# Optimization experiments

Hardware: AMD Instinct MI355X
Metric: run time of the kernel (lower is better)

Reference implementation:

```python
import jax, jax.numpy as jnp
import numpy as np

K = 16  # number of neighbors (module init arg)

def setup_inputs() -> dict:
    key = jax.random.key(0)
    M, D, N = 65536, 16, 64
    x = jax.random.normal(key, (M, D), dtype=jnp.float32)
    # equal-length segments: each point set has M // N points
    segs = jnp.full((N,), M // N, dtype=jnp.int64)
    return {"x": x, "segs": segs}

def reference(x, segs):
    # Segmented kNN graph. Segments are equal-length (static shapes for jit),
    # so the per-segment pairwise distance + top-k becomes a batched op.
    B = segs.shape[0]
    M, D = x.shape
    L = M // B  # points per segment
    pts = x.reshape(B, L, D)
    # squared euclidean distances within each segment: (B, L, L)
    sq = jnp.sum(pts * pts, axis=-1)
    d2 = sq[:, :, None] + sq[:, None, :] - 2.0 * jnp.einsum('bld,bmd->blm', pts, pts)
    # k smallest distances per point (includes self, as in DGL's knn_graph)
    _, idx = jax.lax.top_k(-d2, K)  # idx: (B, L, K), local indices within segment
    offsets = (jnp.arange(B, dtype=idx.dtype) * L)[:, None, None]
    src = (idx + offsets).reshape(-1)                      # neighbor -> global node id
    dst = (jnp.arange(L, dtype=idx.dtype)[None, :, None] + offsets)  # (B, L, 1)
    dst = jnp.broadcast_to(dst, (B, L, K)).reshape(-1)
    # edges point from k-nearest neighbors (predecessors) to each node
    return src, dst
```

## Files before the change

### kernel.cpp

```cpp
#include <hip/hip_runtime.h>
#include <stdint.h>


#define L_SEG 1024
#define M_PTS 65536

typedef __fp16 fp16x2 __attribute__((ext_vector_type(2)));
typedef __fp16 fp16x4 __attribute__((ext_vector_type(4)));
typedef float  f32x4  __attribute__((ext_vector_type(4)));

__device__ __forceinline__ uint32_t umn(uint32_t a, uint32_t b) { return a < b ? a : b; }
__device__ __forceinline__ uint32_t umx(uint32_t a, uint32_t b) { return a > b ? a : b; }

#define CE(arr, i, p) { uint32_t lo = umn(arr[i], arr[p]); uint32_t hi = umx(arr[i], arr[p]); arr[i] = lo; arr[p] = hi; }

__device__ __forceinline__ void clean16(uint32_t* A) {
    #pragma unroll
    for (int j = 8; j > 0; j >>= 1) {
        #pragma unroll
        for (int i = 0; i < 16; ++i) {
            int p = i ^ j;
            if (p > i) CE(A, i, p);
        }
    }
}

__device__ __forceinline__ void sort16(uint32_t* B) {
    #pragma unroll
    for (int p = 1; p < 16; p <<= 1) {
        #pragma unroll
        for (int k = p; k >= 1; k >>= 1) {
            #pragma unroll
            for (int j = (k & (p - 1)); j + k < 16; j += 2 * k) {
                #pragma unroll
                for (int i = 0; i <= ((k - 1 < 15 - j - k) ? k - 1 : 15 - j - k); ++i) {
                    if ((i + j) / (2 * p) == (i + j + k) / (2 * p)) CE(B, i + j, i + j + k);
                }
            }
        }
    }
}

__device__ __forceinline__ void keep16(uint32_t* A, const uint32_t* S) {
    #pragma unroll
    for (int i = 0; i < 16; ++i) A[i] = umn(A[i], S[15 - i]);
    clean16(A);
}

__device__ __forceinline__ void mergeg(uint32_t* A) {
    #pragma unroll
    for (int m = 16; m <= 32; m <<= 1) {
        uint32_t P[16];
        #pragma unroll
        for (int i = 0; i < 16; ++i) P[i] = (uint32_t)__shfl_xor((int)A[15 - i], m, 64);
        #pragma unroll
        for (int i = 0; i < 16; ++i) A[i] = umn(A[i], P[i]);
        clean16(A);
    }
}

__device__ __forceinline__ uint32_t sel4(const uint32_t* A, int g, int v) {
    uint32_t t01 = (g & 1) ? A[4 + v]  : A[v];
    uint32_t t23 = (g & 1) ? A[12 + v] : A[8 + v];
    return (g & 2) ? t23 : t01;
}

__global__ __launch_bounds__(512, 6) void knn_v10_kernel(const float* __restrict__ x,
                                                         int* __restrict__ out) {
    __shared__ __attribute__((aligned(16))) __fp16   sc[L_SEG * 16];
    __shared__ __attribute__((aligned(16))) float    ssq[L_SEG];
    __shared__ __attribute__((aligned(16))) __fp16   sq16[64 * 16];
    __shared__ __attribute__((aligned(16))) uint32_t smerge[64][17];

    const int tid = threadIdx.x;
    const int b   = blockIdx.x;
    const int seg = (b & 7) * 8 + (b >> 7);
    const int qp  = (b >> 3) & 15;
    const float* xseg = x + (size_t)seg * (L_SEG * 16);
    const f32x4* gx4  = (const f32x4*)xseg;

    {
        fp16x4* scv = (fp16x4*)sc;
        #pragma unroll
        for (int i = 0; i < 8; ++i) {
            f32x4 v = gx4[tid + 512 * i];
            union { fp16x2 h2[2]; fp16x4 h4; } u;
            u.h2[0] = __builtin_amdgcn_cvt_pkrtz(-2.0f * v[0], -2.0f * v[1]);
            u.h2[1] = __builtin_amdgcn_cvt_pkrtz(-2.0f * v[2], -2.0f * v[3]);
            scv[tid + 512 * i] = u.h4;
        }
    }
    {
        const int c0 = tid << 1;
        #pragma unroll
        for (int c = 0; c < 2; ++c) {
            float s = 128.0f;
            #pragma unroll
            for (int d = 0; d < 4; ++d) {
                f32x4 v = gx4[(c0 + c) * 4 + d];
                s = __builtin_fmaf(v[0], v[0], s);
                s = __builtin_fmaf(v[1], v[1], s);
                s = __builtin_fmaf(v[2], v[2], s);
                s = __builtin_fmaf(v[3], v[3], s);
            }
            ssq[c0 + c] = s;
        }
    }
    if (tid < 64) {
        const f32x4* qg = gx4 + (size_t)(qp * 64 + tid) * 4;
        fp16x4* dst = (fp16x4*)(sq16 + (size_t)tid * 16);
        #pragma unroll
        for (int d = 0; d < 4; ++d) {
            f32x4 v = qg[d];
            union { fp16x2 h2[2]; fp16x4 h4; } u;
            u.h2[0] = __builtin_amdgcn_cvt_pkrtz(v[0], v[1]);
            u.h2[1] = __builtin_amdgcn_cvt_pkrtz(v[2], v[3]);
            dst[d] = u.h4;
        }
    }
    __syncthreads();

    const int lane = tid & 63;
    const int w    = tid >> 6;
    const int qg   = w & 3;
    const int half = w >> 2;
    const int g    = lane >> 4;
    const int col  = lane & 15;
    const int qloc = qp * 64 + qg * 16 + col;

    const fp16x4 bfrag = *(const fp16x4*)(sq16 + (size_t)(qg * 16 + col) * 16 + g * 4);

    const __fp16* ap  = sc + (size_t)col * 16 + g * 4;
    const float*  sqp = ssq + g * 4;
    const uint32_t vg4 = (uint32_t)(g << 2);
    const int hb = half * 512;

    uint32_t A[16], P[16];
    #pragma unroll
    for (int it = 0; it < 2; ++it) {
        uint32_t* D = it ? P : A;
        const int cb0 = hb + it * 256;
        #pragma unroll
        for (int t = 0; t < 16; ++t) {
            const int cb = cb0 + t * 16;
            fp16x4 af = *(const fp16x4*)(ap + (size_t)cb * 16);
            f32x4  sq = *(const f32x4*)(sqp + cb);
            f32x4 acc = __builtin_amdgcn_mfma_f32_16x16x16f16(af, bfrag, sq, 0, 0, 0);
            const uint32_t ib = (uint32_t)cb + vg4;
            uint32_t k0 = (__float_as_uint(acc[0]) & 0xFFFFFC00u) | ib;
            uint32_t k1 = (__float_as_uint(acc[1]) & 0xFFFFFC00u) | (ib + 1u);
            uint32_t k2 = (__float_as_uint(acc[2]) & 0xFFFFFC00u) | (ib + 2u);
            uint32_t k3 = (__float_as_uint(acc[3]) & 0xFFFFFC00u) | (ib + 3u);
            D[t] = umn(umn(k0, k1), umn(k2, k3));
        }
        sort16(D);
    }
    keep16(A, P);

    mergeg(A);

    const int qb = qg * 16 + col;
    if (half == 1) {
        #pragma unroll
        for (int v = 0; v < 4; ++v) smerge[qb][g * 4 + v] = A[g * 4 + v];
    }
    __syncthreads();
    if (half == 1) return;

    {
        uint32_t Q[16];
        #pragma unroll
        for (int i = 0; i < 16; ++i) Q[i] = smerge[qb][i];
        keep16(A, Q);
    }

    union H8 { f32x4 v[2]; fp16x2 h2[8]; };
    H8 qq;
    {
        const f32x4* qf = (const f32x4*)(sq16 + (size_t)(qg * 16 + col) * 16);
        qq.v[0] = qf[0]; qq.v[1] = qf[1];
    }
    uint32_t R[16];
    #pragma unroll
    for (int v = 0; v < 4; ++v) {
        const uint32_t win = sel4(A, g, v);
        const uint32_t wi  = win & 1023u;
        const uint32_t qbse = wi & ~3u;
        const uint32_t wo  = wi & 3u;
        #pragma unroll
        for (int k = 0; k < 3; ++k) {
            const uint32_t o    = (uint32_t)k + (((uint32_t)k >= wo) ? 1u : 0u);
            const uint32_t pidx = qbse + o;
            H8 cc;
            const f32x4* cf = (const f32x4*)(sc + (size_t)pidx * 16);
            cc.v[0] = cf[0]; cc.v[1] = cf[1];
            float s = 0.0f;
            #pragma unroll
            for (int j = 0; j < 8; ++j) {
#if __has_builtin(__builtin_amdgcn_fdot2)
                s = __builtin_amdgcn_fdot2(cc.h2[j], qq.h2[j], s, false);
#else
                s = __builtin_fmaf((float)cc.h2[j][0], (float)qq.h2[j][0], s);
                s = __builtin_fmaf((float)cc.h2[j][1], (float)qq.h2[j][1], s);
#endif
            }
            const float val = s + ssq[pidx];
            R[v * 3 + k] = (__float_as_uint(val) & 0xFFFFFC00u) | pidx;
        }
    }
    #pragma unroll
    for (int i = 12; i < 16; ++i) R[i] = 0xFFFFFFFFu;
    sort16(R);
    mergeg(R);
    keep16(A, R);

    const int base = seg * L_SEG;
    const int q    = base + qloc;
    int4 sv;
    sv.x = base + (int)(sel4(A, g, 0) & 1023u);
    sv.y = base + (int)(sel4(A, g, 1) & 1023u);
    sv.z = base + (int)(sel4(A, g, 2) & 1023u);
    sv.w = base + (int)(sel4(A, g, 3) & 1023u);
    ((int4*)out)[(size_t)q * 4 + g] = sv;
    ((int4*)out)[(size_t)M_PTS * 4 + (size_t)q * 4 + g] = make_int4(q, q, q, q);
}

extern "C" void kernel_launch(void* const* d_in, const int* in_sizes, int n_in,
                              void* d_out, int out_size, void* d_ws, size_t ws_size,
                              hipStream_t stream) {
    const float* x = (const float*)d_in[0];
    int* out = (int*)d_out;
    (void)d_ws; (void)ws_size;
    knn_v10_kernel<<<dim3(1024), dim3(512), 0, stream>>>(x, out);
}
```

Before: 86.53 us.

## Split kNN into partial top-k kernel over candidate halves plus global merge kernel

Result: slower. 115.4 us (+33.4%).

```diff
diff --git a/kernel.cpp b/kernel.cpp
--- a/kernel.cpp
+++ b/kernel.cpp
@@ -65,29 +65,31 @@
     return (g & 2) ? t23 : t01;
 }
 
-__global__ __launch_bounds__(512, 6) void knn_v10_kernel(const float* __restrict__ x,
-                                                         int* __restrict__ out) {
-    __shared__ __attribute__((aligned(16))) __fp16   sc[L_SEG * 16];
-    __shared__ __attribute__((aligned(16))) float    ssq[L_SEG];
-    __shared__ __attribute__((aligned(16))) __fp16   sq16[64 * 16];
-    __shared__ __attribute__((aligned(16))) uint32_t smerge[64][17];
-
-    const int tid = threadIdx.x;
-    const int b   = blockIdx.x;
-    const int seg = (b & 7) * 8 + (b >> 7);
-    const int qp  = (b >> 3) & 15;
-    const float* xseg = x + (size_t)seg * (L_SEG * 16);
-    const f32x4* gx4  = (const f32x4*)xseg;
+__global__ __launch_bounds__(256, 4) void knn_part_kernel(const float* __restrict__ x,
+                                                          uint32_t* __restrict__ ws) {
+    __shared__ __attribute__((aligned(16))) __fp16 sc[512 * 16];
+    __shared__ __attribute__((aligned(16))) float  ssq[512];
+    __shared__ __attribute__((aligned(16))) __fp16 sq16[64 * 16];
+
+    const int tid   = threadIdx.x;
+    const int b     = blockIdx.x;
+    const int seg   = (b & 7) * 8 + (b >> 8);
+    const int rem   = (b >> 3) & 31;
+    const int slice = rem & 1;
+    const int qp    = rem >> 1;
+    const int cb0   = slice * 512;
+    const f32x4* gx4 = (const f32x4*)(x + (size_t)seg * (L_SEG * 16));
 
     {
         fp16x4* scv = (fp16x4*)sc;
         #pragma unroll
         for (int i = 0; i < 8; ++i) {
-            f32x4 v = gx4[tid + 512 * i];
-            union { fp16x2 h2[2]; fp16x4 h4; } u;
-            u.h2[0] = __builtin_amdgcn_cvt_pkrtz(-2.0f * v[0], -2.0f * v[1]);
-            u.h2[1] = __builtin_amdgcn_cvt_pkrtz(-2.0f * v[2], -2.0f * v[3]);
-            scv[tid + 512 * i] = u.h4;
+            const int u = tid + 256 * i;
+            f32x4 v = gx4[cb0 * 4 + u];
+            union { fp16x2 h2[2]; fp16x4 h4; } uu;
+            uu.h2[0] = __builtin_amdgcn_cvt_pkrtz(-2.0f * v[0], -2.0f * v[1]);
+            uu.h2[1] = __builtin_amdgcn_cvt_pkrtz(-2.0f * v[2], -2.0f * v[3]);
+            scv[u] = uu.h4;
         }
     }
     {
@@ -97,7 +99,7 @@
             float s = 128.0f;
             #pragma unroll
             for (int d = 0; d < 4; ++d) {
-                f32x4 v = gx4[(c0 + c) * 4 + d];
+                f32x4 v = gx4[(cb0 + c0 + c) * 4 + d];
                 s = __builtin_fmaf(v[0], v[0], s);
                 s = __builtin_fmaf(v[1], v[1], s);
                 s = __builtin_fmaf(v[2], v[2], s);
@@ -112,41 +114,38 @@
         #pragma unroll
         for (int d = 0; d < 4; ++d) {
             f32x4 v = qg[d];
-            union { fp16x2 h2[2]; fp16x4 h4; } u;
-            u.h2[0] = __builtin_amdgcn_cvt_pkrtz(v[0], v[1]);
-            u.h2[1] = __builtin_amdgcn_cvt_pkrtz(v[2], v[3]);
-            dst[d] = u.h4;
+            union { fp16x2 h2[2]; fp16x4 h4; } uu;
+            uu.h2[0] = __builtin_amdgcn_cvt_pkrtz(v[0], v[1]);
+            uu.h2[1] = __builtin_amdgcn_cvt_pkrtz(v[2], v[3]);
+            dst[d] = uu.h4;
         }
     }
     __syncthreads();
 
-    const int lane = tid & 63;
-    const int w    = tid >> 6;
-    const int qg   = w & 3;
-    const int half = w >> 2;
-    const int g    = lane >> 4;
-    const int col  = lane & 15;
-    const int qloc = qp * 64 + qg * 16 + col;
-
-    const fp16x4 bfrag = *(const fp16x4*)(sq16 + (size_t)(qg * 16 + col) * 16 + g * 4);
+    const int lane  = tid & 63;
+    const int w     = tid >> 6;
+    const int g     = lane >> 4;
+    const int col   = lane & 15;
+    const int qglob = seg * L_SEG + qp * 64 + w * 16 + col;
+
+    const fp16x4 bfrag = *(const fp16x4*)(sq16 + (size_t)(w * 16 + col) * 16 + g * 4);
 
     const __fp16* ap  = sc + (size_t)col * 16 + g * 4;
     const float*  sqp = ssq + g * 4;
     const uint32_t vg4 = (uint32_t)(g << 2);
-    const int hb = half * 512;
 
     uint32_t A[16], P[16];
     #pragma unroll
-    for (int it = 0; it < 2; ++it) {
-        uint32_t* D = it ? P : A;
-        const int cb0 = hb + it * 256;
+    for (int chain = 0; chain < 2; ++chain) {
+        uint32_t* D = chain ? P : A;
+        const int cc0 = chain * 256;
         #pragma unroll
         for (int t = 0; t < 16; ++t) {
-            const int cb = cb0 + t * 16;
+            const int cb = cc0 + t * 16;
             fp16x4 af = *(const fp16x4*)(ap + (size_t)cb * 16);
             f32x4  sq = *(const f32x4*)(sqp + cb);
             f32x4 acc = __builtin_amdgcn_mfma_f32_16x16x16f16(af, bfrag, sq, 0, 0, 0);
-            const uint32_t ib = (uint32_t)cb + vg4;
+            const uint32_t ib = (uint32_t)(cb0 + cb) + vg4;
             uint32_t k0 = (__float_as_uint(acc[0]) & 0xFFFFFC00u) | ib;
             uint32_t k1 = (__float_as_uint(acc[1]) & 0xFFFFFC00u) | (ib + 1u);
             uint32_t k2 = (__float_as_uint(acc[2]) & 0xFFFFFC00u) | (ib + 2u);
@@ -156,56 +155,70 @@
         sort16(D);
     }
     keep16(A, P);
-
     mergeg(A);
 
-    const int qb = qg * 16 + col;
-    if (half == 1) {
-        #pragma unroll
-        for (int v = 0; v < 4; ++v) smerge[qb][g * 4 + v] = A[g * 4 + v];
-    }
-    __syncthreads();
-    if (half == 1) return;
-
+    uint32_t* wp = ws + ((size_t)qglob * 2 + slice) * 16 + g * 4;
+    uint4 sv;
+    sv.x = sel4(A, g, 0); sv.y = sel4(A, g, 1);
+    sv.z = sel4(A, g, 2); sv.w = sel4(A, g, 3);
+    *(uint4*)wp = sv;
+}
+
+__global__ __launch_bounds__(256, 4) void knn_merge_kernel(const float* __restrict__ x,
+                                                           const uint32_t* __restrict__ ws,
+                                                           int* __restrict__ out) {
+    const int tid  = threadIdx.x;
+    const int lane = tid & 63;
+    const int w    = tid >> 6;
+    const int g    = lane >> 4;
+    const int col  = lane & 15;
+    const int q    = blockIdx.x * 64 + w * 16 + col;
+    const int seg  = q >> 10;
+    const int base = seg << 10;
+    const f32x4* gx4 = (const f32x4*)(x + (size_t)base * 16);
+
+    const uint32_t* wp = ws + (size_t)q * 32;
+    uint32_t A[16], S[16];
     {
-        uint32_t Q[16];
-        #pragma unroll
-        for (int i = 0; i < 16; ++i) Q[i] = smerge[qb][i];
-        keep16(A, Q);
-    }
-
-    union H8 { f32x4 v[2]; fp16x2 h2[8]; };
-    H8 qq;
-    {
-        const f32x4* qf = (const f32x4*)(sq16 + (size_t)(qg * 16 + col) * 16);
-        qq.v[0] = qf[0]; qq.v[1] = qf[1];
-    }
+        const uint4* wv = (const uint4*)wp;
+        #pragma unroll
+        for (int i = 0; i < 4; ++i) {
+            uint4 v = wv[i];
+            A[i * 4 + 0] = v.x; A[i * 4 + 1] = v.y; A[i * 4 + 2] = v.z; A[i * 4 + 3] = v.w;
+        }
+        #pragma unroll
+        for (int i = 0; i < 4; ++i) {
+            uint4 v = wv[4 + i];
+            S[i * 4 + 0] = v.x; S[i * 4 + 1] = v.y; S[i * 4 + 2] = v.z; S[i * 4 + 3] = v.w;
+        }
+    }
+    keep16(A, S);
+
+    const f32x4* qr = gx4 + (size_t)(q - base) * 4;
+    const f32x4 qf0 = qr[0], qf1 = qr[1], qf2 = qr[2], qf3 = qr[3];
     uint32_t R[16];
     #pragma unroll
     for (int v = 0; v < 4; ++v) {
-        const uint32_t win = sel4(A, g, v);
-        const uint32_t wi  = win & 1023u;
-        const uint32_t qbse = wi & ~3u;
+        const uint32_t wi  = sel4(A, g, v) & 1023u;
+        const uint32_t qb2 = wi & ~3u;
         const uint32_t wo  = wi & 3u;
         #pragma unroll
         for (int k = 0; k < 3; ++k) {
             const uint32_t o    = (uint32_t)k + (((uint32_t)k >= wo) ? 1u : 0u);
-            const uint32_t pidx = qbse + o;
-            H8 cc;
-            const f32x4* cf = (const f32x4*)(sc + (size_t)pidx * 16);
-            cc.v[0] = cf[0]; cc.v[1] = cf[1];
-            float s = 0.0f;
+            const uint32_t pidx = qb2 + o;
+            const f32x4* cr = gx4 + (size_t)pidx * 4;
+            float s = 128.0f;
             #pragma unroll
-            for (int j = 0; j < 8; ++j) {
-#if __has_builtin(__builtin_amdgcn_fdot2)
-                s = __builtin_amdgcn_fdot2(cc.h2[j], qq.h2[j], s, false);
-#else
-                s = __builtin_fmaf((float)cc.h2[j][0], (float)qq.h2[j][0], s);
-                s = __builtin_fmaf((float)cc.h2[j][1], (float)qq.h2[j][1], s);
-#endif
+            for (int d = 0; d < 4; ++d) {
+                f32x4 cv = cr[d];
+                f32x4 qv = (d == 0) ? qf0 : (d == 1) ? qf1 : (d == 2) ? qf2 : qf3;
+                #pragma unroll
+                for (int e = 0; e < 4; ++e) {
+                    float t = __builtin_fmaf(qv[e], -2.0f, cv[e]);
+                    s = __builtin_fmaf(cv[e], t, s);
+                }
             }
-            const float val = s + ssq[pidx];
-            R[v * 3 + k] = (__float_as_uint(val) & 0xFFFFFC00u) | pidx;
+            R[v * 3 + k] = (__float_as_uint(s) & 0xFFFFFC00u) | pidx;
         }
     }
     #pragma unroll
@@ -214,8 +227,6 @@
     mergeg(R);
     keep16(A, R);
 
-    const int base = seg * L_SEG;
-    const int q    = base + qloc;
     int4 sv;
     sv.x = base + (int)(sel4(A, g, 0) & 1023u);
     sv.y = base + (int)(sel4(A, g, 1) & 1023u);
@@ -230,6 +241,7 @@
                               hipStream_t stream) {
     const float* x = (const float*)d_in[0];
     int* out = (int*)d_out;
-    (void)d_ws; (void)ws_size;
-    knn_v10_kernel<<<dim3(1024), dim3(512), 0, stream>>>(x, out);
-}
+    uint32_t* ws = (uint32_t*)d_ws;
+    knn_part_kernel<<<dim3(2048), dim3(256), 0, stream>>>(x, ws);
+    knn_merge_kernel<<<dim3(1024), dim3(256), 0, stream>>>(x, ws, out);
+}
```
